# Optimization experiments

Measured on AMD Instinct MI355X. Metric: run time of the kernel, lower is better.

The kernel has to match this reference:

```python
import jax, jax.numpy as jnp
import numpy as np

KH, KW = 3, 3
K_TERMS = KH * KW + 1  # ones (linear/bias) + 9 shifted patches
# pair indices (i<=j), same ordering as the original layer
_PAIRS = [(i, j) for i in range(K_TERMS) for j in range(i, K_TERMS)]
II = np.array([p[0] for p in _PAIRS])  # [55]
JJ = np.array([p[1] for p in _PAIRS])  # [55]


def setup_inputs() -> dict:
    key = jax.random.key(0)
    k1, k2 = jax.random.split(key)
    B, H, W, C, O = 8, 56, 56, 64, 128
    inputs = jax.random.normal(k1, (B, H, W, C), dtype=jnp.float32)
    # glorot-ish scale for the [1,1,55,C,O] conv3d kernel (squeezed to [55,C,O])
    fan = 55 * C + O
    kernel = jax.random.normal(k2, (55, C, O), dtype=jnp.float32) * jnp.sqrt(2.0 / fan)
    return {"inputs": inputs, "kernel": kernel}


def reference(inputs, kernel):
    B, H, W, C = inputs.shape
    # 'same' padding for stride 1: pad_total = k - 1, asymmetric split as in TF
    ph, pw = KH - 1, KW - 1
    xp = jnp.pad(inputs, ((0, 0), (ph // 2, ph - ph // 2), (pw // 2, pw - pw // 2), (0, 0)))
    # im2col-style shifted slices, row-major over (r, c) like i//kw, i%kw
    shifts = jnp.stack(
        [xp[:, r:r + H, c:c + W, :] for r in range(KH) for c in range(KW)],
        axis=3,
    )  # [B,H,W,9,C]
    ones = jnp.ones((B, H, W, 1, C), dtype=inputs.dtype)
    S = jnp.concatenate([ones, shifts], axis=3)  # [B,H,W,10,C]
    # pairwise quadratic features (includes bias = ones*ones and linear = ones*shift)
    quad = S[:, :, :, II, :] * S[:, :, :, JJ, :]  # [B,H,W,55,C]
    # 1x1x1 conv3d over depth-55 == contraction over (pair, channel)
    return jnp.einsum('bhwpc,pco->bhwo', quad, kernel)  # [B,H,W,O]
```

## Files before the change

kernel.cpp:

```cpp
#include <hip/hip_runtime.h>


#define CB 8
#define CH 56
#define CW 56
#define CC 64
#define CO 128
#define RS 72

typedef __attribute__((ext_vector_type(8))) _Float16 v8hf;
typedef __attribute__((ext_vector_type(16))) float f16f;

__device__ constexpr int PII[55] = {0,0,0,0,0,0,0,0,0,0, 1,1,1,1,1,1,1,1,1, 2,2,2,2,2,2,2,2,
                                    3,3,3,3,3,3,3, 4,4,4,4,4,4, 5,5,5,5,5, 6,6,6,6, 7,7,7, 8,8, 9};
__device__ constexpr int PJJ[55] = {0,1,2,3,4,5,6,7,8,9, 1,2,3,4,5,6,7,8,9, 2,3,4,5,6,7,8,9,
                                    3,4,5,6,7,8,9, 4,5,6,7,8,9, 5,6,7,8,9, 6,7,8,9, 7,8,9, 8,9, 9};

__global__ __launch_bounds__(256) void prep_kernel(const float* __restrict__ K,
                                                   _Float16* __restrict__ Bt) {
  __shared__ float tile[CC * CO];
  const int p = blockIdx.x;
  const int t = threadIdx.x;
  const float* src = K + (size_t)p * CC * CO;
#pragma unroll
  for (int e = 0; e < 8; ++e) {
    const int idx = t * 4 + e * 1024;
    *(float4*)&tile[idx] = *(const float4*)&src[idx];
  }
  __syncthreads();
  const int n = t & 127;
  const int kh = t >> 7;
  _Float16 ov[32];
#pragma unroll
  for (int k = 0; k < 32; ++k)
    ov[k] = (_Float16)tile[(kh * 32 + k) * CO + n];
  _Float16* dst = Bt + ((size_t)p * CO + n) * CC + kh * 32;
#pragma unroll
  for (int g = 0; g < 4; ++g)
    *(v8hf*)(dst + g * 8) = *(const v8hf*)&ov[g * 8];
}

__global__ __launch_bounds__(256, 1) void quad_kernel(const float* __restrict__ in,
                                                      const _Float16* __restrict__ Bt,
                                                      float* __restrict__ out) {
  __shared__ _Float16 rowsH[4][64][RS];

  const int t = threadIdx.x;
  const int b = blockIdx.x / (CH / 2);
  const int h0 = (blockIdx.x % (CH / 2)) * 2;

  {
    const int col = t >> 2;
    const int cg = (t & 3) * 16;
    const int w = col - 1;
#pragma unroll
    for (int r = 0; r < 4; ++r) {
      const int hh = h0 + r - 1;
      const bool valid = (hh >= 0) && (hh < CH) && (w >= 0) && (w < CW);
      float4 v0 = make_float4(0.f, 0.f, 0.f, 0.f), v1 = v0, v2 = v0, v3 = v0;
      if (valid) {
        const float* s = in + (((size_t)(b * CH + hh)) * CW + w) * CC + cg;
        v0 = *(const float4*)(s);
        v1 = *(const float4*)(s + 4);
        v2 = *(const float4*)(s + 8);
        v3 = *(const float4*)(s + 12);
      }
      _Float16 pv[16];
      pv[0] = (_Float16)v0.x;  pv[1] = (_Float16)v0.y;  pv[2] = (_Float16)v0.z;  pv[3] = (_Float16)v0.w;
      pv[4] = (_Float16)v1.x;  pv[5] = (_Float16)v1.y;  pv[6] = (_Float16)v1.z;  pv[7] = (_Float16)v1.w;
      pv[8] = (_Float16)v2.x;  pv[9] = (_Float16)v2.y;  pv[10] = (_Float16)v2.z; pv[11] = (_Float16)v2.w;
      pv[12] = (_Float16)v3.x; pv[13] = (_Float16)v3.y; pv[14] = (_Float16)v3.z; pv[15] = (_Float16)v3.w;
      _Float16* d = &rowsH[r][col][cg];
      *(v8hf*)(d) = *(const v8hf*)&pv[0];
      *(v8hf*)(d + 8) = *(const v8hf*)&pv[8];
    }
  }

  const int lane = t & 63;
  const int nq = t >> 6;
  const int ml = lane & 31;
  const int hk = lane >> 5;
  const int h8 = hk * 8;

  f16f acc0, acc1, acc2, acc3;
#pragma unroll
  for (int r = 0; r < 16; ++r) { acc0[r] = 0.f; acc1[r] = 0.f; acc2[r] = 0.f; acc3[r] = 0.f; }

  const _Float16* Bn = Bt + ((size_t)(nq * 32 + ml)) * CC + h8;
  const v8hf vone = {1, 1, 1, 1, 1, 1, 1, 1};

  v8hf ring[11];
#pragma unroll
  for (int p = 0; p < 11; ++p)
    ring[p] = *(const v8hf*)(Bn + (size_t)p * (CO * CC));

  __syncthreads();

#pragma unroll 1
  for (int ks = 0; ks < 4; ++ks) {
    const int koff = ks * 16 + h8;
    v8hf s0[9], s1[9], s2[9], s3[9];
#pragma unroll
    for (int tt = 0; tt < 9; ++tt) {
      const int rr = tt / 3, sc = tt % 3;
      const int c0 = ml + sc;
      int c1 = 32 + ml + sc; c1 = c1 > 63 ? 63 : c1;
      s0[tt] = *(const v8hf*)&rowsH[rr][c0][koff];
      s1[tt] = *(const v8hf*)&rowsH[rr][c1][koff];
      s2[tt] = *(const v8hf*)&rowsH[rr + 1][c0][koff];
      s3[tt] = *(const v8hf*)&rowsH[rr + 1][c1][koff];
    }
    const int ksn = (ks < 3) ? ks + 1 : 3;
#pragma unroll
    for (int p = 0; p < 55; ++p) {
      const v8hf bb = ring[p % 11];
      {
        const int p2 = (p < 44) ? p + 11 : p - 44;
        const _Float16* ba = Bn + (size_t)p2 * (CO * CC) + ((p < 44) ? ks : ksn) * 16;
        ring[p % 11] = *(const v8hf*)ba;
      }
      const int pi = PII[p], pj = PJJ[p];
      v8hf a0, a1, a2, a3;
      if (pi == 0) {
        if (pj == 0) { a0 = vone; a1 = vone; a2 = vone; a3 = vone; }
        else { a0 = s0[pj - 1]; a1 = s1[pj - 1]; a2 = s2[pj - 1]; a3 = s3[pj - 1]; }
      } else {
        a0 = s0[pi - 1] * s0[pj - 1];
        a1 = s1[pi - 1] * s1[pj - 1];
        a2 = s2[pi - 1] * s2[pj - 1];
        a3 = s3[pi - 1] * s3[pj - 1];
      }
      acc0 = __builtin_amdgcn_mfma_f32_32x32x16_f16(a0, bb, acc0, 0, 0, 0);
      acc1 = __builtin_amdgcn_mfma_f32_32x32x16_f16(a1, bb, acc1, 0, 0, 0);
      acc2 = __builtin_amdgcn_mfma_f32_32x32x16_f16(a2, bb, acc2, 0, 0, 0);
      acc3 = __builtin_amdgcn_mfma_f32_32x32x16_f16(a3, bb, acc3, 0, 0, 0);
    }
  }

  const size_t rowstride = (size_t)CW * CO;
  float* ob0 = out + ((size_t)(b * CH + h0) * CW) * CO + nq * 32 + ml;
  float* ob1 = ob0 + rowstride;
#pragma unroll
  for (int r = 0; r < 16; ++r) {
    const int wp = (r & 3) + 8 * (r >> 2) + 4 * hk;
    ob0[(size_t)wp * CO] = acc0[r];
    ob1[(size_t)wp * CO] = acc2[r];
  }
#pragma unroll
  for (int r = 0; r < 12; ++r) {
    const int wp = 32 + (r & 3) + 8 * (r >> 2) + 4 * hk;
    ob0[(size_t)wp * CO] = acc1[r];
    ob1[(size_t)wp * CO] = acc3[r];
  }
}

extern "C" void kernel_launch(void* const* d_in, const int* in_sizes, int n_in,
                              void* d_out, int out_size, void* d_ws, size_t ws_size,
                              hipStream_t stream) {
  const float* in = (const float*)d_in[0];
  const float* K = (const float*)d_in[1];
  float* out = (float*)d_out;
  _Float16* Bt = (_Float16*)d_ws;
  (void)in_sizes; (void)n_in; (void)out_size; (void)ws_size;

  prep_kernel<<<55, 256, 0, stream>>>(K, Bt);
  quad_kernel<<<CB * (CH / 2), 256, 0, stream>>>(in, Bt, out);
}
```

Baseline: 97.66 us.

## Process one output row per block to cut registers and raise occupancy

Each block now computes a single output row instead of two. This halves the accumulators, the shifted-patch registers and the B prefetch ring (11 to 5), and launch bounds now allow two blocks per CU. The grid doubles to 448 blocks, which fills the CUs better and gives more latency hiding. In exchange each B fragment loaded from global memory is reused across half as many MFMAs, and the shared-row loading is less amortised (3 rows per output row instead of 4 per 2), so global and L2 traffic rises.

```diff
diff --git a/kernel.cpp b/kernel.cpp
--- a/kernel.cpp
+++ b/kernel.cpp
@@ -40,22 +40,22 @@
     *(v8hf*)(dst + g * 8) = *(const v8hf*)&ov[g * 8];
 }
 
-__global__ __launch_bounds__(256, 1) void quad_kernel(const float* __restrict__ in,
+__global__ __launch_bounds__(256, 2) void quad_kernel(const float* __restrict__ in,
                                                       const _Float16* __restrict__ Bt,
                                                       float* __restrict__ out) {
-  __shared__ _Float16 rowsH[4][64][RS];
+  __shared__ _Float16 rowsH[3][64][RS];
 
   const int t = threadIdx.x;
-  const int b = blockIdx.x / (CH / 2);
-  const int h0 = (blockIdx.x % (CH / 2)) * 2;
+  const int b = blockIdx.x / CH;
+  const int hrow = blockIdx.x % CH;
 
   {
     const int col = t >> 2;
     const int cg = (t & 3) * 16;
     const int w = col - 1;
 #pragma unroll
-    for (int r = 0; r < 4; ++r) {
-      const int hh = h0 + r - 1;
+    for (int r = 0; r < 3; ++r) {
+      const int hh = hrow + r - 1;
       const bool valid = (hh >= 0) && (hh < CH) && (w >= 0) && (w < CW);
       float4 v0 = make_float4(0.f, 0.f, 0.f, 0.f), v1 = v0, v2 = v0, v3 = v0;
       if (valid) {
@@ -82,16 +82,16 @@
   const int hk = lane >> 5;
   const int h8 = hk * 8;
 
-  f16f acc0, acc1, acc2, acc3;
+  f16f acc0, acc1;
 #pragma unroll
-  for (int r = 0; r < 16; ++r) { acc0[r] = 0.f; acc1[r] = 0.f; acc2[r] = 0.f; acc3[r] = 0.f; }
+  for (int r = 0; r < 16; ++r) { acc0[r] = 0.f; acc1[r] = 0.f; }
 
   const _Float16* Bn = Bt + ((size_t)(nq * 32 + ml)) * CC + h8;
   const v8hf vone = {1, 1, 1, 1, 1, 1, 1, 1};
 
-  v8hf ring[11];
+  v8hf ring[5];
 #pragma unroll
-  for (int p = 0; p < 11; ++p)
+  for (int p = 0; p < 5; ++p)
     ring[p] = *(const v8hf*)(Bn + (size_t)p * (CO * CC));
 
   __syncthreads();
@@ -99,7 +99,7 @@
 #pragma unroll 1
   for (int ks = 0; ks < 4; ++ks) {
     const int koff = ks * 16 + h8;
-    v8hf s0[9], s1[9], s2[9], s3[9];
+    v8hf s0[9], s1[9];
 #pragma unroll
     for (int tt = 0; tt < 9; ++tt) {
       const int rr = tt / 3, sc = tt % 3;
@@ -107,50 +107,40 @@
       int c1 = 32 + ml + sc; c1 = c1 > 63 ? 63 : c1;
       s0[tt] = *(const v8hf*)&rowsH[rr][c0][koff];
       s1[tt] = *(const v8hf*)&rowsH[rr][c1][koff];
-      s2[tt] = *(const v8hf*)&rowsH[rr + 1][c0][koff];
-      s3[tt] = *(const v8hf*)&rowsH[rr + 1][c1][koff];
     }
     const int ksn = (ks < 3) ? ks + 1 : 3;
 #pragma unroll
     for (int p = 0; p < 55; ++p) {
-      const v8hf bb = ring[p % 11];
+      const v8hf bb = ring[p % 5];
       {
-        const int p2 = (p < 44) ? p + 11 : p - 44;
-        const _Float16* ba = Bn + (size_t)p2 * (CO * CC) + ((p < 44) ? ks : ksn) * 16;
-        ring[p % 11] = *(const v8hf*)ba;
+        const int p2 = (p < 50) ? p + 5 : p - 50;
+        const _Float16* ba = Bn + (size_t)p2 * (CO * CC) + ((p < 50) ? ks : ksn) * 16;
+        ring[p % 5] = *(const v8hf*)ba;
       }
       const int pi = PII[p], pj = PJJ[p];
-      v8hf a0, a1, a2, a3;
+      v8hf a0, a1;
       if (pi == 0) {
-        if (pj == 0) { a0 = vone; a1 = vone; a2 = vone; a3 = vone; }
-        else { a0 = s0[pj - 1]; a1 = s1[pj - 1]; a2 = s2[pj - 1]; a3 = s3[pj - 1]; }
+        if (pj == 0) { a0 = vone; a1 = vone; }
+        else { a0 = s0[pj - 1]; a1 = s1[pj - 1]; }
       } else {
         a0 = s0[pi - 1] * s0[pj - 1];
         a1 = s1[pi - 1] * s1[pj - 1];
-        a2 = s2[pi - 1] * s2[pj - 1];
-        a3 = s3[pi - 1] * s3[pj - 1];
       }
       acc0 = __builtin_amdgcn_mfma_f32_32x32x16_f16(a0, bb, acc0, 0, 0, 0);
       acc1 = __builtin_amdgcn_mfma_f32_32x32x16_f16(a1, bb, acc1, 0, 0, 0);
-      acc2 = __builtin_amdgcn_mfma_f32_32x32x16_f16(a2, bb, acc2, 0, 0, 0);
-      acc3 = __builtin_amdgcn_mfma_f32_32x32x16_f16(a3, bb, acc3, 0, 0, 0);
     }
   }
 
-  const size_t rowstride = (size_t)CW * CO;
-  float* ob0 = out + ((size_t)(b * CH + h0) * CW) * CO + nq * 32 + ml;
-  float* ob1 = ob0 + rowstride;
+  float* ob = out + ((size_t)(b * CH + hrow) * CW) * CO + nq * 32 + ml;
 #pragma unroll
   for (int r = 0; r < 16; ++r) {
     const int wp = (r & 3) + 8 * (r >> 2) + 4 * hk;
-    ob0[(size_t)wp * CO] = acc0[r];
-    ob1[(size_t)wp * CO] = acc2[r];
+    ob[(size_t)wp * CO] = acc0[r];
   }
 #pragma unroll
   for (int r = 0; r < 12; ++r) {
     const int wp = 32 + (r & 3) + 8 * (r >> 2) + 4 * hk;
-    ob0[(size_t)wp * CO] = acc1[r];
-    ob1[(size_t)wp * CO] = acc3[r];
+    ob[(size_t)wp * CO] = acc1[r];
   }
 }
 
@@ -164,5 +154,5 @@
   (void)in_sizes; (void)n_in; (void)out_size; (void)ws_size;
 
   prep_kernel<<<55, 256, 0, stream>>>(K, Bt);
-  quad_kernel<<<CB * (CH / 2), 256, 0, stream>>>(in, Bt, out);
+  quad_kernel<<<CB * CH, 256, 0, stream>>>(in, Bt, out);
 }
```

After: 119.1 us. 22.0% more time.
